# Optimization experiments

Measured on AMD Instinct MI355X. Metric: run time of the kernel, lower is better.

The kernel has to match this reference:

```python
import jax, jax.numpy as jnp
import numpy as np

W_TEMPORAL = 0.5
W_SPATIAL = 0.5
SIGMA = 2.0


def setup_inputs() -> dict:
    key = jax.random.key(0)
    ks = jax.random.split(key, 12)
    L, B, F, S, Y = 1024, 32, 24, 12, 48
    return {
        "f": jax.random.normal(ks[0], (L, B, F), jnp.float32),
        "s": jax.random.normal(ks[1], (L, B, S), jnp.float32),
        "fs": jax.random.normal(ks[2], (L, B, F, S), jnp.float32),
        "ff": jax.random.normal(ks[3], (L, B, F, F), jnp.float32),
        "ss": jax.random.normal(ks[4], (L, B, S, S), jnp.float32),
        "fs_t": jax.random.normal(ks[5], (L, B, F, S), jnp.float32),
        "sf_t": jax.random.normal(ks[6], (L, B, S, F), jnp.float32),
        "f_labels": jax.random.randint(ks[7], (L, B), 0, F),
        "s_labels": jax.random.randint(ks[8], (L, B), 0, S),
        "y_labels": jax.random.randint(ks[9], (L, B), 0, Y),
        "mask": jnp.ones((L, B), jnp.bool_),
        "y_to_f_index": jax.random.randint(ks[10], (Y,), 0, F),
        "y_to_s_index": jax.random.randint(ks[11], (Y,), 0, S),
    }


def _message_weights(L, dtype):
    # W_past[t, i] = K(i, t) / t   for i < t (row 0 all zeros)
    # W_future[t, i] = K(t, i) / (L-1-t) for i > t (last row all zeros)
    t = jnp.arange(L, dtype=dtype)
    diff = t[None, :] - t[:, None]  # [t, i] = i - t
    K = jnp.exp(-(diff * diff) / (2.0 * SIGMA * SIGMA))
    past = jnp.where(diff < 0, K, 0.0) / jnp.maximum(t, 1.0)[:, None]
    fut = jnp.where(diff > 0, K, 0.0) / jnp.maximum((L - 1.0) - t, 1.0)[:, None]
    return past, fut


def _pass_messages(W, pot, L, B):
    # pot: (L*B, C) laid out row-major over (L, B)
    C = pot.shape[1]
    out = jnp.einsum("ti,ibc->tbc", W, pot.reshape(L, B, C))
    return out.reshape(L * B, C)


def _masked_ce(logits, labels, maskf):
    logp = jax.nn.log_softmax(logits, axis=1)
    nll = -jnp.take_along_axis(logp, labels[:, None], axis=1)[:, 0]
    return jnp.sum(nll * maskf) / jnp.sum(maskf)


def reference(f, s, fs, ff, ss, fs_t, sf_t, f_labels, s_labels, y_labels,
              mask, y_to_f_index, y_to_s_index):
    L, B, F = f.shape
    S = s.shape[2]
    N = L * B
    orig_f = f.reshape(N, F)
    orig_s = s.reshape(N, S)
    fl = f_labels.reshape(N)
    sl = s_labels.reshape(N)
    yl = y_labels.reshape(N)
    maskf = mask.reshape(N).astype(f.dtype)

    loss = _masked_ce(orig_f, fl, maskf) + _masked_ce(orig_s, sl, maskf)

    # structured loss: NLL applied to a product of probabilities (as in source)
    fy = jax.nn.softmax(orig_f, axis=1)[:, y_to_f_index]
    sy = jax.nn.softmax(orig_s, axis=1)[:, y_to_s_index]
    y = fy * sy
    struct = -jnp.take_along_axis(y, yl[:, None], axis=1)[:, 0]
    loss = loss + jnp.sum(struct * maskf) / jnp.sum(maskf)

    flat_fs = fs.reshape(N, F, S)
    flat_ff = ff.reshape(N, F, F)
    flat_ss = ss.reshape(N, S, S)
    flat_fs_t = fs_t.reshape(N, F, S)
    flat_sf_t = sf_t.reshape(N, S, F)

    W_past, W_fut = _message_weights(L, f.dtype)

    prev_f = orig_f
    prev_s = orig_s
    num_iterations = 1  # training path (evaluate=False)
    for _ in range(num_iterations):
        f_mp = _pass_messages(W_past, prev_f, L, B)
        f_mf = _pass_messages(W_fut, prev_f, L, B)
        s_mp = _pass_messages(W_past, prev_s, L, B)
        s_mf = _pass_messages(W_fut, prev_s, L, B)

        next_f = (orig_f
                  + W_TEMPORAL * jnp.einsum("nf,nfg->ng", f_mp, flat_ff)
                  + W_TEMPORAL * jnp.einsum("nfg,ng->nf", flat_ff, f_mf)
                  + W_TEMPORAL * jnp.einsum("ns,nsf->nf", s_mp, flat_sf_t)
                  + W_TEMPORAL * jnp.einsum("nfs,ns->nf", flat_fs_t, s_mf)
                  + W_SPATIAL * jnp.einsum("nfs,ns->nf", flat_fs, prev_s))
        next_s = (orig_s
                  + W_TEMPORAL * jnp.einsum("ns,nst->nt", s_mp, flat_ss)
                  + W_TEMPORAL * jnp.einsum("nst,nt->ns", flat_ss, s_mf)
                  + W_TEMPORAL * jnp.einsum("nf,nfs->ns", f_mp, flat_fs_t)
                  + W_TEMPORAL * jnp.einsum("nsf,nf->ns", flat_sf_t, f_mf)
                  + W_SPATIAL * jnp.einsum("nf,nfs->ns", prev_f, flat_fs))
        prev_f = jax.nn.softmax(next_f, axis=1)
        prev_s = jax.nn.softmax(next_s, axis=1)

    loss = loss + _masked_ce(next_f, fl, maskf) + _masked_ce(next_s, sl, maskf)

    f_out = prev_f.reshape(L, B, F)
    s_out = prev_s.reshape(L, B, S)
    return (f_out, s_out, loss)
```

## Files before the change

kernel.cpp:

```cpp
#include <hip/hip_runtime.h>
#include <math.h>

#define L_C 1024
#define B_C 32
#define F_C 24
#define S_C 12
#define N_C (L_C*B_C)
#define DWIN 20
#define GRID 768
#define NGRP (N_C/4)
#define GRP_F4 1584
#define BUF_F4 1600

__global__ void msg_kernel(const float* __restrict__ x, float* __restrict__ mp,
                           float* __restrict__ mf, int C) {
    int idx = blockIdx.x * 256 + threadIdx.x;
    int stride = B_C * C;
    int total = N_C * C;
    if (idx >= total) return;
    int t = idx / stride;
    float accp = 0.f, accf = 0.f;
    #pragma unroll
    for (int d = 1; d <= DWIN; ++d) {
        float w = expf(-0.125f * (float)(d * d));
        if (t >= d)        accp += w * x[idx - d * stride];
        if (t + d < L_C)   accf += w * x[idx + d * stride];
    }
    mp[idx] = accp / fmaxf((float)t, 1.0f);
    mf[idx] = accf / fmaxf((float)(L_C - 1 - t), 1.0f);
}

__device__ inline float segred_max(float v) {
    #pragma unroll
    for (int o = 16; o >= 1; o >>= 1) v = fmaxf(v, __shfl_xor(v, o, 32));
    return v;
}
__device__ inline float segred_sum(float v) {
    #pragma unroll
    for (int o = 16; o >= 1; o >>= 1) v += __shfl_xor(v, o, 32);
    return v;
}

__global__ __launch_bounds__(256, 3) void fuse_kernel(
    const float* __restrict__ f,  const float* __restrict__ s,
    const float* __restrict__ fs, const float* __restrict__ ff,
    const float* __restrict__ ss, const float* __restrict__ fst,
    const float* __restrict__ sft,
    const int* __restrict__ fl, const int* __restrict__ sl,
    const int* __restrict__ yl, const int* __restrict__ y2f,
    const int* __restrict__ y2s,
    const float* __restrict__ fmp, const float* __restrict__ fmf,
    const float* __restrict__ smp, const float* __restrict__ smf,
    float* __restrict__ outf, float* __restrict__ outs,
    float* __restrict__ part)
{
    __shared__ float4 L4[2*BUF_F4];
    float* Lf = (float*)L4;
    char*  LB = (char*)L4;

    const int tid  = threadIdx.x;
    const int bid  = blockIdx.x;
    const int w    = tid >> 6;
    const int lane = tid & 63;

    const char *p0,*p1,*p2,*p3,*p4,*p5,*p6;
    int s0,s1,s2,s3,s4,s5,s6;
    {
        auto mk = [&](int j, const char*& P, int& S) {
            int i = tid + 256*j; if (i > GRP_F4-1) i = GRP_F4-1;
            const float* base; int off, gsz;
            if (i < 576)       { base = ff;  off = i;        gsz = 576; }
            else if (i < 864)  { base = fs;  off = i - 576;  gsz = 288; }
            else if (i < 1152) { base = fst; off = i - 864;  gsz = 288; }
            else if (i < 1440) { base = sft; off = i - 1152; gsz = 288; }
            else               { base = ss;  off = i - 1440; gsz = 144; }
            P = (const char*)base + ((size_t)bid*gsz + off)*16;
            S = gsz * GRID * 16;
        };
        mk(0,p0,s0); mk(1,p1,s1); mk(2,p2,s2); mk(3,p3,s3);
        mk(4,p4,s4); mk(5,p5,s5); mk(6,p6,s6);
    }

    const int wbase = w*64*16;

    #define ISSUE(J, PJ) \
        __builtin_amdgcn_global_load_lds( \
            (const __attribute__((address_space(1))) void*)(PJ), \
            (__attribute__((address_space(3))) void*)(LB + (co) + (J)*256*16 + wbase), \
            16, 0, 0)
    #define STAGE(coff) do { int co = (coff); \
        ISSUE(0,p0); ISSUE(1,p1); ISSUE(2,p2); \
        ISSUE(3,p3); ISSUE(4,p4); ISSUE(5,p5); \
        if (tid < 64) { ISSUE(6,p6); } \
        p0+=s0; p1+=s1; p2+=s2; p3+=s3; p4+=s4; p5+=s5; p6+=s6; \
    } while(0)

    const int niter = (NGRP - bid + GRID - 1) / GRID;

    STAGE(0);
    __syncthreads();

    float lsum = 0.f;
    int cur = 0;

    for (int it = 0; it < niter; ++it) {
        if (it + 1 < niter) STAGE((cur^1) * (BUF_F4*16));

        const int nu = __builtin_amdgcn_readfirstlane(4*(bid + it*GRID) + w);

        const float* Lb   = Lf + cur*(BUF_F4*4);
        const float* sFF  = Lb +        w*576;
        const float* sFS  = Lb + 2304 + w*288;
        const float* sFST = Lb + 3456 + w*288;
        const float* sSFT = Lb + 4608 + w*288;
        const float* sSS  = Lb + 5760 + w*144;

        const float* vmpf = fmp + (size_t)nu*24;
        const float* vmff = fmf + (size_t)nu*24;
        const float* vmps = smp + (size_t)nu*12;
        const float* vmfs = smf + (size_t)nu*12;
        const float* vF   = f   + (size_t)nu*24;
        const float* vS   = s   + (size_t)nu*12;

        const bool isF    = lane < 32;
        const bool active = (lane < 24) | (lane >= 32 && lane < 44);
        const int gg = (lane < 24) ? lane : 23;
        const int tt = ((lane & 31) < 12) ? (lane & 31) : 11;

        float acc = 0.f;
        {
            const float* pp = isF ? (sFF + gg) : (sFST + tt);
            const int st    = isF ? 24 : 12;
            #pragma unroll
            for (int k = 0; k < 24; ++k) acc += vmpf[k] * pp[k*st];
        }
        {
            const float4* q  = (const float4*)(isF ? (sFF + gg*24) : (sSFT + tt*24));
            const float4* v4 = (const float4*)vmff;
            #pragma unroll
            for (int k = 0; k < 6; ++k) {
                float4 a = q[k], b = v4[k];
                acc += a.x*b.x + a.y*b.y + a.z*b.z + a.w*b.w;
            }
        }
        {
            const float* pp = isF ? (sSFT + gg) : (sSS + tt);
            const int st    = isF ? 24 : 12;
            #pragma unroll
            for (int k = 0; k < 12; ++k) acc += vmps[k] * pp[k*st];
        }
        {
            const float4* q  = (const float4*)(isF ? (sFST + gg*12) : (sSS + tt*12));
            const float4* v4 = (const float4*)vmfs;
            #pragma unroll
            for (int k = 0; k < 3; ++k) {
                float4 a = q[k], b = v4[k];
                acc += a.x*b.x + a.y*b.y + a.z*b.z + a.w*b.w;
            }
        }
        if (isF) {
            const float4* q  = (const float4*)(sFS + gg*12);
            const float4* v4 = (const float4*)vS;
            #pragma unroll
            for (int k = 0; k < 3; ++k) {
                float4 a = q[k], b = v4[k];
                acc += a.x*b.x + a.y*b.y + a.z*b.z + a.w*b.w;
            }
        } else {
            const float* pp = sFS + tt;
            #pragma unroll
            for (int k = 0; k < 24; ++k) acc += vF[k] * pp[k*12];
        }

        float fval = 0.f;
        if (lane < 24)                    fval = vF[lane];
        else if (lane >= 32 && lane < 44) fval = vS[lane - 32];

        float nx = fval + 0.5f * acc;
        float xo = active ? fval : -INFINITY;
        float xn = active ? nx   : -INFINITY;

        float mo = segred_max(xo);
        float eo = expf(xo - mo);
        float so = segred_sum(eo);
        float lse_o = mo + logf(so);

        float mn = segred_max(xn);
        float en = expf(xn - mn);
        float sn = segred_sum(en);
        float pr = en / sn;
        float lse_n = mn + logf(sn);

        const size_t n = (size_t)nu;
        if (lane < 24)                    outf[n*24 + lane]        = pr;
        else if (lane >= 32 && lane < 44) outs[n*12 + (lane - 32)] = pr;

        const int fln = fl[nu], sln = sl[nu], yln = yl[nu];
        const int yfi = y2f[yln], ysi = y2s[yln];
        float lse_o_s = __shfl(lse_o, 32, 64);
        float lse_n_s = __shfl(lse_n, 32, 64);
        float vf_fl   = __shfl(xo, fln, 64);
        float vs_sl   = __shfl(xo, 32 + sln, 64);
        float nf_fl   = __shfl(xn, fln, 64);
        float ns_sl   = __shfl(xn, 32 + sln, 64);
        float vf_y    = __shfl(xo, yfi, 64);
        float vs_y    = __shfl(xo, 32 + ysi, 64);
        if (lane == 0) {
            float ce1 = lse_o   - vf_fl;
            float ce2 = lse_o_s - vs_sl;
            float stc = -expf(vf_y - lse_o) * expf(vs_y - lse_o_s);
            float ce3 = lse_n   - nf_fl;
            float ce4 = lse_n_s - ns_sl;
            lsum += ce1 + ce2 + stc + ce3 + ce4;
        }

        __syncthreads();
        cur ^= 1;
    }

    if (lane == 0) part[bid*4 + w] = lsum;
    #undef STAGE
    #undef ISSUE
}

__global__ void loss_reduce(const float* __restrict__ part, float* __restrict__ out) {
    __shared__ float sm[256];
    float a = 0.f;
    for (int i = threadIdx.x; i < GRID*4; i += 256) a += part[i];
    sm[threadIdx.x] = a;
    __syncthreads();
    for (int o = 128; o >= 1; o >>= 1) {
        if ((int)threadIdx.x < o) sm[threadIdx.x] += sm[threadIdx.x + o];
        __syncthreads();
    }
    if (threadIdx.x == 0) out[0] = sm[0] * (1.0f / (float)N_C);
}

extern "C" void kernel_launch(void* const* d_in, const int* in_sizes, int n_in,
                              void* d_out, int out_size, void* d_ws, size_t ws_size,
                              hipStream_t stream) {
    (void)in_sizes; (void)n_in; (void)out_size; (void)ws_size;

    const float* f   = (const float*)d_in[0];
    const float* s   = (const float*)d_in[1];
    const float* fs  = (const float*)d_in[2];
    const float* ff  = (const float*)d_in[3];
    const float* ss  = (const float*)d_in[4];
    const float* fst = (const float*)d_in[5];
    const float* sft = (const float*)d_in[6];
    const int* fl  = (const int*)d_in[7];
    const int* sl  = (const int*)d_in[8];
    const int* yl  = (const int*)d_in[9];
    const int* y2f = (const int*)d_in[11];
    const int* y2s = (const int*)d_in[12];

    float* ws   = (float*)d_ws;
    float* fmp  = ws;
    float* fmf  = fmp + (size_t)N_C * F_C;
    float* smp  = fmf + (size_t)N_C * F_C;
    float* smf  = smp + (size_t)N_C * S_C;
    float* part = smf + (size_t)N_C * S_C;

    float* outf = (float*)d_out;
    float* outs = outf + (size_t)N_C * F_C;
    float* outl = outs + (size_t)N_C * S_C;

    msg_kernel<<<(N_C * F_C) / 256, 256, 0, stream>>>(f, fmp, fmf, F_C);
    msg_kernel<<<(N_C * S_C) / 256, 256, 0, stream>>>(s, smp, smf, S_C);
    fuse_kernel<<<GRID, 256, 0, stream>>>(f, s, fs, ff, ss, fst, sft,
                                          fl, sl, yl, y2f, y2s,
                                          fmp, fmf, smp, smf,
                                          outf, outs, part);
    loss_reduce<<<1, 256, 0, stream>>>(part, outl);
}
```

Before: 89.23 us.

## Split original-logit loss into separate kernel and restructure fuse to single-wave blocks

Moves the cross-entropy terms on the original f/s logits into a new standalone kernel with a per-block tree reduction. The fuse kernel becomes one-wave blocks over a strided row mapping with register-prefetched LDS staging instead of async global-to-LDS double buffering and block barriers. Column-wise (strided) matrix reads now go to global memory and only row-wise reads use LDS. This removes barrier stalls and shrinks LDS use to raise occupancy, at the cost of an extra launch, rereading f and s, and uncoalesced-style global column loads.

```diff
diff --git a/kernel.cpp b/kernel.cpp
--- a/kernel.cpp
+++ b/kernel.cpp
@@ -7,10 +7,8 @@
 #define S_C 12
 #define N_C (L_C*B_C)
 #define DWIN 20
-#define GRID 768
-#define NGRP (N_C/4)
-#define GRP_F4 1584
-#define BUF_F4 1600
+#define GRID_F 4096
+#define ITERS 8
 
 __global__ void msg_kernel(const float* __restrict__ x, float* __restrict__ mp,
                            float* __restrict__ mf, int C) {
@@ -41,79 +39,116 @@
     return v;
 }
 
-__global__ __launch_bounds__(256, 3) void fuse_kernel(
+__global__ __launch_bounds__(256) void lossA_kernel(
+    const float* __restrict__ f, const float* __restrict__ s,
+    const int* __restrict__ fl, const int* __restrict__ sl,
+    const int* __restrict__ yl, const int* __restrict__ y2f,
+    const int* __restrict__ y2s, float* __restrict__ part2)
+{
+    __shared__ float sm[256];
+    const int n = blockIdx.x * 256 + threadIdx.x;
+
+    const float4* pf = (const float4*)(f + (size_t)n*24);
+    float4 a0 = pf[0], a1 = pf[1], a2 = pf[2], a3 = pf[3], a4 = pf[4], a5 = pf[5];
+    const float4* ps = (const float4*)(s + (size_t)n*12);
+    float4 b0 = ps[0], b1 = ps[1], b2 = ps[2];
+
+    #define MX4(v) fmaxf(fmaxf(v.x,v.y),fmaxf(v.z,v.w))
+    float mF = fmaxf(fmaxf(fmaxf(MX4(a0),MX4(a1)),fmaxf(MX4(a2),MX4(a3))),
+                     fmaxf(MX4(a4),MX4(a5)));
+    float mS = fmaxf(MX4(b0), fmaxf(MX4(b1), MX4(b2)));
+    #undef MX4
+    #define SE4(v,m) (expf(v.x-m)+expf(v.y-m)+expf(v.z-m)+expf(v.w-m))
+    float sF = SE4(a0,mF)+SE4(a1,mF)+SE4(a2,mF)+SE4(a3,mF)+SE4(a4,mF)+SE4(a5,mF);
+    float sS = SE4(b0,mS)+SE4(b1,mS)+SE4(b2,mS);
+    #undef SE4
+    float lseF = mF + logf(sF);
+    float lseS = mS + logf(sS);
+
+    const int fln = fl[n], sln = sl[n], yln = yl[n];
+    float f_fl = f[(size_t)n*24 + fln];
+    float s_sl = s[(size_t)n*12 + sln];
+    float f_y  = f[(size_t)n*24 + y2f[yln]];
+    float s_y  = s[(size_t)n*12 + y2s[yln]];
+
+    float v = (lseF - f_fl) + (lseS - s_sl)
+            - expf(f_y - lseF) * expf(s_y - lseS);
+
+    sm[threadIdx.x] = v;
+    __syncthreads();
+    for (int o = 128; o >= 1; o >>= 1) {
+        if ((int)threadIdx.x < o) sm[threadIdx.x] += sm[threadIdx.x + o];
+        __syncthreads();
+    }
+    if (threadIdx.x == 0) part2[blockIdx.x] = sm[0];
+}
+
+__global__ __launch_bounds__(64, 4) void fuse_kernel(
     const float* __restrict__ f,  const float* __restrict__ s,
     const float* __restrict__ fs, const float* __restrict__ ff,
     const float* __restrict__ ss, const float* __restrict__ fst,
     const float* __restrict__ sft,
     const int* __restrict__ fl, const int* __restrict__ sl,
-    const int* __restrict__ yl, const int* __restrict__ y2f,
-    const int* __restrict__ y2s,
     const float* __restrict__ fmp, const float* __restrict__ fmf,
     const float* __restrict__ smp, const float* __restrict__ smf,
     float* __restrict__ outf, float* __restrict__ outs,
     float* __restrict__ part)
 {
-    __shared__ float4 L4[2*BUF_F4];
-    float* Lf = (float*)L4;
-    char*  LB = (char*)L4;
-
-    const int tid  = threadIdx.x;
+    __shared__ float4 LDS4[7*64];
+    float* Lf = (float*)LDS4;
+
+    const int lane = threadIdx.x;
     const int bid  = blockIdx.x;
-    const int w    = tid >> 6;
-    const int lane = tid & 63;
 
     const char *p0,*p1,*p2,*p3,*p4,*p5,*p6;
     int s0,s1,s2,s3,s4,s5,s6;
     {
         auto mk = [&](int j, const char*& P, int& S) {
-            int i = tid + 256*j; if (i > GRP_F4-1) i = GRP_F4-1;
-            const float* base; int off, gsz;
-            if (i < 576)       { base = ff;  off = i;        gsz = 576; }
-            else if (i < 864)  { base = fs;  off = i - 576;  gsz = 288; }
-            else if (i < 1152) { base = fst; off = i - 864;  gsz = 288; }
-            else if (i < 1440) { base = sft; off = i - 1152; gsz = 288; }
-            else               { base = ss;  off = i - 1440; gsz = 144; }
-            P = (const char*)base + ((size_t)bid*gsz + off)*16;
-            S = gsz * GRID * 16;
+            int i = 64*j + lane; if (i > 395) i = 395;
+            const float* base; int off, rowf4;
+            if (i < 144)      { base = ff;  off = i;       rowf4 = 144; }
+            else if (i < 216) { base = fs;  off = i - 144; rowf4 = 72;  }
+            else if (i < 288) { base = fst; off = i - 216; rowf4 = 72;  }
+            else if (i < 360) { base = sft; off = i - 288; rowf4 = 72;  }
+            else              { base = ss;  off = i - 360; rowf4 = 36;  }
+            P = (const char*)base + ((size_t)bid*rowf4 + off)*16;
+            S = rowf4 * GRID_F * 16;
         };
         mk(0,p0,s0); mk(1,p1,s1); mk(2,p2,s2); mk(3,p3,s3);
         mk(4,p4,s4); mk(5,p5,s5); mk(6,p6,s6);
     }
 
-    const int wbase = w*64*16;
-
-    #define ISSUE(J, PJ) \
-        __builtin_amdgcn_global_load_lds( \
-            (const __attribute__((address_space(1))) void*)(PJ), \
-            (__attribute__((address_space(3))) void*)(LB + (co) + (J)*256*16 + wbase), \
-            16, 0, 0)
-    #define STAGE(coff) do { int co = (coff); \
-        ISSUE(0,p0); ISSUE(1,p1); ISSUE(2,p2); \
-        ISSUE(3,p3); ISSUE(4,p4); ISSUE(5,p5); \
-        if (tid < 64) { ISSUE(6,p6); } \
-        p0+=s0; p1+=s1; p2+=s2; p3+=s3; p4+=s4; p5+=s5; p6+=s6; \
-    } while(0)
-
-    const int niter = (NGRP - bid + GRID - 1) / GRID;
-
-    STAGE(0);
-    __syncthreads();
+    float4 r0,r1,r2,r3,r4,r5,r6;
+    #define LOADR() do { \
+        r0 = *(const float4*)p0; p0 += s0; r1 = *(const float4*)p1; p1 += s1; \
+        r2 = *(const float4*)p2; p2 += s2; r3 = *(const float4*)p3; p3 += s3; \
+        r4 = *(const float4*)p4; p4 += s4; r5 = *(const float4*)p5; p5 += s5; \
+        r6 = *(const float4*)p6; p6 += s6; } while(0)
+    #define WRITER() do { \
+        LDS4[0*64+lane]=r0; LDS4[1*64+lane]=r1; LDS4[2*64+lane]=r2; \
+        LDS4[3*64+lane]=r3; LDS4[4*64+lane]=r4; LDS4[5*64+lane]=r5; \
+        LDS4[6*64+lane]=r6; } while(0)
+
+    const bool isF    = lane < 32;
+    const bool active = (lane < 24) | (lane >= 32 && lane < 44);
+    const int gg = (lane < 24) ? lane : 23;
+    const int tt = ((lane & 31) < 12) ? (lane & 31) : 11;
+
+    const float4* rowP2 = (const float4*)(isF ? (Lf + gg*24) : (Lf + 1152 + tt*24));
+    const float4* rowP4 = (const float4*)(isF ? (Lf + 864 + gg*12) : (Lf + 1440 + tt*12));
+    const float4* rowP5 = (const float4*)(Lf + 576 + gg*12);
+    const int cs1 = isF ? 96 : 48;
+    const int cs3 = isF ? 96 : 48;
+
+    LOADR();
+    WRITER();
+    LOADR();
 
     float lsum = 0.f;
-    int cur = 0;
-
-    for (int it = 0; it < niter; ++it) {
-        if (it + 1 < niter) STAGE((cur^1) * (BUF_F4*16));
-
-        const int nu = __builtin_amdgcn_readfirstlane(4*(bid + it*GRID) + w);
-
-        const float* Lb   = Lf + cur*(BUF_F4*4);
-        const float* sFF  = Lb +        w*576;
-        const float* sFS  = Lb + 2304 + w*288;
-        const float* sFST = Lb + 3456 + w*288;
-        const float* sSFT = Lb + 4608 + w*288;
-        const float* sSS  = Lb + 5760 + w*144;
+
+    #pragma unroll 1
+    for (int it = 0; it < ITERS; ++it) {
+        const int nu = bid + it*GRID_F;
 
         const float* vmpf = fmp + (size_t)nu*24;
         const float* vmff = fmf + (size_t)nu*24;
@@ -122,54 +157,49 @@
         const float* vF   = f   + (size_t)nu*24;
         const float* vS   = s   + (size_t)nu*12;
 
-        const bool isF    = lane < 32;
-        const bool active = (lane < 24) | (lane >= 32 && lane < 44);
-        const int gg = (lane < 24) ? lane : 23;
-        const int tt = ((lane & 31) < 12) ? (lane & 31) : 11;
-
         float acc = 0.f;
+
         {
-            const float* pp = isF ? (sFF + gg) : (sFST + tt);
-            const int st    = isF ? 24 : 12;
-            #pragma unroll
-            for (int k = 0; k < 24; ++k) acc += vmpf[k] * pp[k*st];
+            const char* q = isF ? (const char*)(ff  + (size_t)nu*576 + gg)
+                                : (const char*)(fst + (size_t)nu*288 + tt);
+            #pragma unroll
+            for (int k = 0; k < 24; ++k) {
+                acc += vmpf[k] * *(const float*)q;
+                q += cs1;
+            }
+        }
+        #pragma unroll
+        for (int k = 0; k < 6; ++k) {
+            float4 a = rowP2[k];
+            acc += a.x*vmff[4*k] + a.y*vmff[4*k+1] + a.z*vmff[4*k+2] + a.w*vmff[4*k+3];
         }
         {
-            const float4* q  = (const float4*)(isF ? (sFF + gg*24) : (sSFT + tt*24));
-            const float4* v4 = (const float4*)vmff;
-            #pragma unroll
-            for (int k = 0; k < 6; ++k) {
-                float4 a = q[k], b = v4[k];
-                acc += a.x*b.x + a.y*b.y + a.z*b.z + a.w*b.w;
-            }
-        }
-        {
-            const float* pp = isF ? (sSFT + gg) : (sSS + tt);
-            const int st    = isF ? 24 : 12;
-            #pragma unroll
-            for (int k = 0; k < 12; ++k) acc += vmps[k] * pp[k*st];
-        }
-        {
-            const float4* q  = (const float4*)(isF ? (sFST + gg*12) : (sSS + tt*12));
-            const float4* v4 = (const float4*)vmfs;
+            const char* q = isF ? (const char*)(sft + (size_t)nu*288 + gg)
+                                : (const char*)(ss  + (size_t)nu*144 + tt);
+            #pragma unroll
+            for (int k = 0; k < 12; ++k) {
+                acc += vmps[k] * *(const float*)q;
+                q += cs3;
+            }
+        }
+        #pragma unroll
+        for (int k = 0; k < 3; ++k) {
+            float4 a = rowP4[k];
+            acc += a.x*vmfs[4*k] + a.y*vmfs[4*k+1] + a.z*vmfs[4*k+2] + a.w*vmfs[4*k+3];
+        }
+        if (isF) {
             #pragma unroll
             for (int k = 0; k < 3; ++k) {
-                float4 a = q[k], b = v4[k];
-                acc += a.x*b.x + a.y*b.y + a.z*b.z + a.w*b.w;
-            }
-        }
-        if (isF) {
-            const float4* q  = (const float4*)(sFS + gg*12);
-            const float4* v4 = (const float4*)vS;
-            #pragma unroll
-            for (int k = 0; k < 3; ++k) {
-                float4 a = q[k], b = v4[k];
-                acc += a.x*b.x + a.y*b.y + a.z*b.z + a.w*b.w;
+                float4 a = rowP5[k];
+                acc += a.x*vS[4*k] + a.y*vS[4*k+1] + a.z*vS[4*k+2] + a.w*vS[4*k+3];
             }
         } else {
-            const float* pp = sFS + tt;
-            #pragma unroll
-            for (int k = 0; k < 24; ++k) acc += vF[k] * pp[k*12];
+            const char* q = (const char*)(fs + (size_t)nu*288 + tt);
+            #pragma unroll
+            for (int k = 0; k < 24; ++k) {
+                acc += vF[k] * *(const float*)q;
+                q += 48;
+            }
         }
 
         float fval = 0.f;
@@ -177,13 +207,7 @@
         else if (lane >= 32 && lane < 44) fval = vS[lane - 32];
 
         float nx = fval + 0.5f * acc;
-        float xo = active ? fval : -INFINITY;
-        float xn = active ? nx   : -INFINITY;
-
-        float mo = segred_max(xo);
-        float eo = expf(xo - mo);
-        float so = segred_sum(eo);
-        float lse_o = mo + logf(so);
+        float xn = active ? nx : -INFINITY;
 
         float mn = segred_max(xn);
         float en = expf(xn - mn);
@@ -191,42 +215,34 @@
         float pr = en / sn;
         float lse_n = mn + logf(sn);
 
-        const size_t n = (size_t)nu;
-        if (lane < 24)                    outf[n*24 + lane]        = pr;
-        else if (lane >= 32 && lane < 44) outs[n*12 + (lane - 32)] = pr;
-
-        const int fln = fl[nu], sln = sl[nu], yln = yl[nu];
-        const int yfi = y2f[yln], ysi = y2s[yln];
-        float lse_o_s = __shfl(lse_o, 32, 64);
+        const size_t nn = (size_t)nu;
+        if (lane < 24)                    outf[nn*24 + lane]        = pr;
+        else if (lane >= 32 && lane < 44) outs[nn*12 + (lane - 32)] = pr;
+
+        const int fln = fl[nu], sln = sl[nu];
         float lse_n_s = __shfl(lse_n, 32, 64);
-        float vf_fl   = __shfl(xo, fln, 64);
-        float vs_sl   = __shfl(xo, 32 + sln, 64);
         float nf_fl   = __shfl(xn, fln, 64);
         float ns_sl   = __shfl(xn, 32 + sln, 64);
-        float vf_y    = __shfl(xo, yfi, 64);
-        float vs_y    = __shfl(xo, 32 + ysi, 64);
-        if (lane == 0) {
-            float ce1 = lse_o   - vf_fl;
-            float ce2 = lse_o_s - vs_sl;
-            float stc = -expf(vf_y - lse_o) * expf(vs_y - lse_o_s);
-            float ce3 = lse_n   - nf_fl;
-            float ce4 = lse_n_s - ns_sl;
-            lsum += ce1 + ce2 + stc + ce3 + ce4;
-        }
-
-        __syncthreads();
-        cur ^= 1;
-    }
-
-    if (lane == 0) part[bid*4 + w] = lsum;
-    #undef STAGE
-    #undef ISSUE
-}
-
-__global__ void loss_reduce(const float* __restrict__ part, float* __restrict__ out) {
+        if (lane == 0) lsum += (lse_n - nf_fl) + (lse_n_s - ns_sl);
+
+        if (it + 1 < ITERS) {
+            WRITER();
+            if (it + 2 < ITERS) LOADR();
+        }
+    }
+
+    if (lane == 0) part[bid] = lsum;
+    #undef LOADR
+    #undef WRITER
+}
+
+__global__ void loss_reduce(const float* __restrict__ part,
+                            const float* __restrict__ part2,
+                            float* __restrict__ out) {
     __shared__ float sm[256];
     float a = 0.f;
-    for (int i = threadIdx.x; i < GRID*4; i += 256) a += part[i];
+    for (int i = threadIdx.x; i < GRID_F; i += 256) a += part[i];
+    for (int i = threadIdx.x; i < N_C/256; i += 256) a += part2[i];
     sm[threadIdx.x] = a;
     __syncthreads();
     for (int o = 128; o >= 1; o >>= 1) {
@@ -254,12 +270,13 @@
     const int* y2f = (const int*)d_in[11];
     const int* y2s = (const int*)d_in[12];
 
-    float* ws   = (float*)d_ws;
-    float* fmp  = ws;
-    float* fmf  = fmp + (size_t)N_C * F_C;
-    float* smp  = fmf + (size_t)N_C * F_C;
-    float* smf  = smp + (size_t)N_C * S_C;
-    float* part = smf + (size_t)N_C * S_C;
+    float* ws    = (float*)d_ws;
+    float* fmp   = ws;
+    float* fmf   = fmp  + (size_t)N_C * F_C;
+    float* smp   = fmf  + (size_t)N_C * F_C;
+    float* smf   = smp  + (size_t)N_C * S_C;
+    float* part  = smf  + (size_t)N_C * S_C;
+    float* part2 = part + GRID_F;
 
     float* outf = (float*)d_out;
     float* outs = outf + (size_t)N_C * F_C;
@@ -267,9 +284,10 @@
 
     msg_kernel<<<(N_C * F_C) / 256, 256, 0, stream>>>(f, fmp, fmf, F_C);
     msg_kernel<<<(N_C * S_C) / 256, 256, 0, stream>>>(s, smp, smf, S_C);
-    fuse_kernel<<<GRID, 256, 0, stream>>>(f, s, fs, ff, ss, fst, sft,
-                                          fl, sl, yl, y2f, y2s,
-                                          fmp, fmf, smp, smf,
-                                          outf, outs, part);
-    loss_reduce<<<1, 256, 0, stream>>>(part, outl);
-}
+    lossA_kernel<<<N_C / 256, 256, 0, stream>>>(f, s, fl, sl, yl, y2f, y2s, part2);
+    fuse_kernel<<<GRID_F, 64, 0, stream>>>(f, s, fs, ff, ss, fst, sft,
+                                           fl, sl,
+                                           fmp, fmf, smp, smf,
+                                           outf, outs, part);
+    loss_reduce<<<1, 256, 0, stream>>>(part, part2, outl);
+}
```

Measured after the change: 155.3 us. +74.0%, slower.
